# Optimization experiments

Measured on AMD Instinct MI355X. Metric: run time of the kernel, lower is better.

## Reference

```python
import jax, jax.numpy as jnp
import numpy as np

D_MODEL = 1024
N_HEADS = 16
HEAD_DIM = D_MODEL // N_HEADS
MAX_REL = 1024
BATCH = 4
SEQ = 1024


def setup_inputs() -> dict:
    key = jax.random.key(0)
    ks = jax.random.split(key, 12)
    f32 = jnp.float32
    scale = 0.02
    inp = {
        "query": jax.random.normal(ks[0], (BATCH, SEQ, D_MODEL), f32),
        "key": jax.random.normal(ks[1], (BATCH, SEQ, D_MODEL), f32),
        "value": jax.random.normal(ks[2], (BATCH, SEQ, D_MODEL), f32),
        # causal mask: 1 indicates positions to mask (strict upper triangle)
        "attention_mask": jnp.triu(jnp.ones((SEQ, SEQ), jnp.int32), k=1)[None, None],
        "Wq": jax.random.normal(ks[3], (D_MODEL, D_MODEL), f32) * scale,
        "bq": jnp.zeros((D_MODEL,), f32),
        "Wk": jax.random.normal(ks[4], (D_MODEL, D_MODEL), f32) * scale,
        "bk": jnp.zeros((D_MODEL,), f32),
        "Wv": jax.random.normal(ks[5], (D_MODEL, D_MODEL), f32) * scale,
        "bv": jnp.zeros((D_MODEL,), f32),
        "rel_tab": jax.random.normal(ks[6], (MAX_REL, D_MODEL), f32) * scale,
        "Wo": jax.random.normal(ks[7], (D_MODEL, D_MODEL), f32) * scale,
        "bo": jnp.zeros((D_MODEL,), f32),
    }
    return inp


def _relative_positions(rel_tab, seq_len):
    # Mirrors get_relative_positions with max_len = MAX_REL (static ints).
    pad_n = max(seq_len - MAX_REL, 0)
    start = max(MAX_REL - seq_len, 0)
    tail = rel_tab[start:MAX_REL]  # (min(seq_len, MAX_REL), D)
    if pad_n > 0:
        head = jnp.tile(rel_tab[0:1], (pad_n, 1))
        return jnp.concatenate([head, tail], axis=0)
    return tail  # (seq_len, D)


def _skew(pos_raw):
    # pos_raw: (B, H, S, S). Music-Transformer skew trick:
    # pad one column on the left, reshape, drop first row, reshape back.
    B, H, Sq, Sk = pos_raw.shape
    padded = jnp.pad(pos_raw, ((0, 0), (0, 0), (0, 0), (1, 0)))  # (B,H,Sq,Sk+1)
    t = padded.reshape(-1, Sk + 1, Sq)
    return t[:, 1:].reshape(B, H, Sq, Sk)


def reference(query, key, value, attention_mask, Wq, bq, Wk, bk, Wv, bv, rel_tab, Wo, bo):
    B, Sq, D = query.shape
    Sk = key.shape[-2]
    H, hd = N_HEADS, HEAD_DIM

    q = query @ Wq + bq
    k = key @ Wk + bk
    v = value @ Wv + bv
    rel = _relative_positions(rel_tab, Sk)  # (Sk, D)

    # split heads -> (B, H, S, hd); rel -> (H, Sk, hd)
    qh = q.reshape(B, Sq, H, hd).transpose(0, 2, 1, 3)
    kh = k.reshape(B, Sk, H, hd).transpose(0, 2, 1, 3)
    vh = v.reshape(B, Sk, H, hd).transpose(0, 2, 1, 3)
    rh = rel.reshape(Sk, H, hd).transpose(1, 0, 2)

    content = jnp.einsum('bhqd,bhkd->bhqk', qh, kh)
    pos_raw = jnp.einsum('bhqd,hkd->bhqk', qh, rh)
    pos = _skew(pos_raw)

    scale = 1.0 / np.sqrt(hd).astype(np.float32)
    scores = (content + pos) * scale
    scores = jnp.where(attention_mask == 1, jnp.float32(-1e9), scores)
    weights = jax.nn.softmax(scores, axis=-1)

    out = jnp.einsum('bhqk,bhkd->bhqd', weights, vh)
    out = out.transpose(0, 2, 1, 3).reshape(B, Sq, D)
    return out @ Wo + bo
```

## Files before the change

kernel.cpp:

```cpp
#include <hip/hip_runtime.h>
#include <cstddef>
#include <cstdint>


typedef __attribute__((ext_vector_type(8))) short bf16x8;
typedef __attribute__((ext_vector_type(4))) float f32x4;
typedef __attribute__((ext_vector_type(4))) unsigned int u32x4;

using u16 = unsigned short;
using u32 = unsigned int;

#define QSCALE (0.125f * 1.44269504089f)

__device__ __forceinline__ f32x4 mfma16(bf16x8 a, bf16x8 b, f32x4 c) {
  return __builtin_amdgcn_mfma_f32_16x16x32_bf16(a, b, c, 0, 0, 0);
}
__device__ __forceinline__ u32 fbits(float f) {
  union { float f; u32 u; } v; v.f = f; return v.u;
}
__device__ __forceinline__ float uif(u32 u) {
  union { u32 u; float f; } v; v.u = u; return v.f;
}
__device__ __forceinline__ u16 f2b(float f) { return (u16)((fbits(f) + 0x8000u) >> 16); }
__device__ __forceinline__ u32 pack2(float a, float b) {
  return ((fbits(a) + 0x8000u) >> 16) | ((fbits(b) + 0x8000u) & 0xffff0000u);
}
__device__ __forceinline__ float b2f(u16 u) {
  union { u32 i; float f; } v; v.i = ((u32)u) << 16; return v.f;
}
__device__ __forceinline__ float exp2_fast(float x) {
  float r; asm("v_exp_f32 %0, %1" : "=v"(r) : "v"(x)); return r;
}
__device__ __forceinline__ void gload16(const void* g, void* l) {
  __builtin_amdgcn_global_load_lds(
      (const __attribute__((address_space(1))) u32*)g,
      (__attribute__((address_space(3))) u32*)l, 16, 0, 0);
}

__global__ __launch_bounds__(256) void cvt_qkv(
    const float* __restrict__ a0, const float* __restrict__ a1,
    const float* __restrict__ a2, u16* __restrict__ o0,
    u16* __restrict__ o1, u16* __restrict__ o2) {
  int z = blockIdx.y;
  const float* src = (z == 0) ? a0 : (z == 1) ? a1 : a2;
  u16* dst = (z == 0) ? o0 : (z == 1) ? o1 : o2;
  size_t i = ((size_t)blockIdx.x * 256 + threadIdx.x) * 4;
  f32x4 v = *(const f32x4*)(src + i);
  uint2 pk; pk.x = pack2(v[0], v[1]); pk.y = pack2(v[2], v[3]);
  *(uint2*)(dst + i) = pk;
}

__global__ __launch_bounds__(256) void prep(
    const float* __restrict__ Wq, const float* __restrict__ Wk,
    const float* __restrict__ Wv, const float* __restrict__ rel,
    u16* __restrict__ WqT, u16* __restrict__ WkT, u16* __restrict__ WvT,
    u16* __restrict__ relb) {
  __shared__ __align__(16) u16 tile[64][65];
  int z = blockIdx.z;
  if (z == 3) {
    int blk = blockIdx.y * 16 + blockIdx.x;
    size_t base = (size_t)blk * 4096;
#pragma unroll
    for (int e = 0; e < 4; e++) {
      size_t idx = base + e * 1024 + threadIdx.x * 4;
      f32x4 v = *(const f32x4*)(rel + idx);
      uint2 pk; pk.x = pack2(v[0], v[1]); pk.y = pack2(v[2], v[3]);
      *(uint2*)(relb + idx) = pk;
    }
    return;
  }
  const float* W = (z == 0) ? Wq : (z == 1) ? Wk : Wv;
  u16* T = (z == 0) ? WqT : (z == 1) ? WkT : WvT;
  float sc = (z == 0) ? QSCALE : 1.0f;
  int k0 = blockIdx.x * 64, n0 = blockIdx.y * 64;
  for (int e = threadIdx.x; e < 4096; e += 256) {
    int r = e >> 6, c = e & 63;
    tile[r][c] = f2b(sc * W[(size_t)(k0 + r) * 1024 + n0 + c]);
  }
  __syncthreads();
  for (int e = threadIdx.x; e < 4096; e += 256) {
    int r = e >> 6, c = e & 63;
    T[(size_t)(n0 + r) * 1024 + k0 + c] = tile[c][r];
  }
}

__global__ __launch_bounds__(256) void transpose_wo(
    const float* __restrict__ W, u16* __restrict__ T) {
  __shared__ __align__(16) u16 tile[64][65];
  int k0 = blockIdx.x * 64, n0 = blockIdx.y * 64;
  for (int e = threadIdx.x; e < 4096; e += 256) {
    int r = e >> 6, c = e & 63;
    tile[r][c] = f2b(W[(size_t)(k0 + r) * 1024 + n0 + c]);
  }
  __syncthreads();
  for (int e = threadIdx.x; e < 4096; e += 256) {
    int r = e >> 6, c = e & 63;
    T[(size_t)(n0 + r) * 1024 + k0 + c] = tile[c][r];
  }
}

__device__ __forceinline__ void gemm_epilogue(
    f32x4 (&acc)[4][4], const float* __restrict__ bias, float bscale,
    void* __restrict__ Cv, int layout, int m0, int n0, int wr, int wc,
    int quad, int ln) {
#pragma unroll
  for (int ct = 0; ct < 4; ct++) {
    int n = n0 + wc + 16 * ct + ln;
    float bs = bscale * bias[n];
#pragma unroll
    for (int rt = 0; rt < 4; rt++) {
#pragma unroll
      for (int r = 0; r < 4; r++) {
        int m = m0 + wr + 16 * rt + quad * 4 + r;
        float v = acc[rt][ct][r] + bs;
        if (layout == 0) {
          ((float*)Cv)[(size_t)m * 1024 + n] = v;
        } else {
          int b_ = m >> 10, s = m & 1023, h = n >> 6, d = n & 63;
          size_t idx = (layout == 1)
              ? ((size_t)(b_ * 16 + h) * 1024 + s) * 64 + d
              : ((size_t)(b_ * 16 + h) * 64 + d) * 1024 + s;
          ((u16*)Cv)[idx] = f2b(v);
        }
      }
    }
  }
}

__device__ __forceinline__ void gemm_glds_body(
    const u16* __restrict__ A, const u16* __restrict__ Bt,
    const float* __restrict__ bias, float bscale, void* __restrict__ Cv,
    int layout) {
  __shared__ __align__(16) u16 As[128 * 64];
  __shared__ __align__(16) u16 Bs[128 * 64];
  int m0 = blockIdx.x * 128, n0 = blockIdx.y * 128;
  int tid = threadIdx.x;
  int w = tid >> 6, lane = tid & 63, quad = lane >> 4, ln = lane & 15;
  int wr = (w >> 1) * 64, wc = (w & 1) * 64;

  int rowin = lane >> 3;
  int swz = ((lane & 7) ^ rowin) * 8;

  f32x4 acc[4][4];
#pragma unroll
  for (int i = 0; i < 4; i++)
#pragma unroll
    for (int j = 0; j < 4; j++) { acc[i][j][0]=0.f; acc[i][j][1]=0.f; acc[i][j][2]=0.f; acc[i][j][3]=0.f; }

  const u16* aA = A  + (size_t)(m0 + 32 * w + rowin) * 1024 + swz;
  const u16* aB = Bt + (size_t)(n0 + 32 * w + rowin) * 1024 + swz;

  for (int k0 = 0; k0 < 1024; k0 += 64) {
#pragma unroll
    for (int j = 0; j < 4; j++) {
      gload16(aA + k0 + (size_t)(8 * j) * 1024, &As[(32 * w + 8 * j) * 64]);
      gload16(aB + k0 + (size_t)(8 * j) * 1024, &Bs[(32 * w + 8 * j) * 64]);
    }
    __syncthreads();
#pragma unroll
    for (int kk = 0; kk < 64; kk += 32) {
      int sA = (((quad + (kk >> 3)) ^ (ln & 7))) * 8;
      bf16x8 af[4], bfr[4];
#pragma unroll
      for (int rt = 0; rt < 4; rt++)
        af[rt] = *(const bf16x8*)&As[(wr + 16 * rt + ln) * 64 + sA];
#pragma unroll
      for (int ct = 0; ct < 4; ct++)
        bfr[ct] = *(const bf16x8*)&Bs[(wc + 16 * ct + ln) * 64 + sA];
#pragma unroll
      for (int rt = 0; rt < 4; rt++)
#pragma unroll
        for (int ct = 0; ct < 4; ct++)
          acc[rt][ct] = mfma16(af[rt], bfr[ct], acc[rt][ct]);
    }
    __syncthreads();
  }

  gemm_epilogue(acc, bias, bscale, Cv, layout, m0, n0, wr, wc, quad, ln);
}

__device__ __forceinline__ void gemm128_body_f32(
    const float* __restrict__ Av, const u16* __restrict__ Bt,
    const float* __restrict__ bias, float bscale, void* __restrict__ Cv,
    int layout) {
  __shared__ __align__(16) u16 As[128][72];
  __shared__ __align__(16) u16 Bs[128][72];
  int m0 = blockIdx.x * 128, n0 = blockIdx.y * 128;
  int tid = threadIdx.x;
  int w = tid >> 6, lane = tid & 63, quad = lane >> 4, ln = lane & 15;
  int wr = (w >> 1) * 64, wc = (w & 1) * 64;
  int sr = tid >> 1, seg = (tid & 1) * 32;

  f32x4 acc[4][4];
#pragma unroll
  for (int i = 0; i < 4; i++)
#pragma unroll
    for (int j = 0; j < 4; j++) { acc[i][j][0]=0.f; acc[i][j][1]=0.f; acc[i][j][2]=0.f; acc[i][j][3]=0.f; }

  for (int k0 = 0; k0 < 1024; k0 += 64) {
    {
      const float* ap = Av + (size_t)(m0 + sr) * 1024 + k0 + seg;
      u32 pk[16];
#pragma unroll
      for (int j = 0; j < 8; j++) {
        f32x4 v = *(const f32x4*)(ap + 4 * j);
        pk[2 * j]     = pack2(v[0], v[1]);
        pk[2 * j + 1] = pack2(v[2], v[3]);
      }
      u32* d = (u32*)&As[sr][seg];
#pragma unroll
      for (int j = 0; j < 4; j++) *(u32x4*)(d + 4 * j) = *(u32x4*)(pk + 4 * j);
    }
    {
      const u16* bp = Bt + (size_t)(n0 + sr) * 1024 + k0 + seg;
#pragma unroll
      for (int j = 0; j < 4; j++)
        *(bf16x8*)&Bs[sr][seg + 8 * j] = *(const bf16x8*)(bp + 8 * j);
    }
    __syncthreads();
#pragma unroll
    for (int kk = 0; kk < 64; kk += 32) {
      bf16x8 af[4], bfr[4];
#pragma unroll
      for (int rt = 0; rt < 4; rt++)
        af[rt] = *(const bf16x8*)&As[wr + 16 * rt + ln][kk + quad * 8];
#pragma unroll
      for (int ct = 0; ct < 4; ct++)
        bfr[ct] = *(const bf16x8*)&Bs[wc + 16 * ct + ln][kk + quad * 8];
#pragma unroll
      for (int rt = 0; rt < 4; rt++)
#pragma unroll
        for (int ct = 0; ct < 4; ct++)
          acc[rt][ct] = mfma16(af[rt], bfr[ct], acc[rt][ct]);
    }
    __syncthreads();
  }

  gemm_epilogue(acc, bias, bscale, Cv, layout, m0, n0, wr, wc, quad, ln);
}

__global__ __launch_bounds__(256) void gemm_qkv_f32(
    const float* q, const float* k, const float* v, const u16* WT,
    const float* bq, const float* bk, const float* bv,
    u16* Qp, u16* Kp, u16* Vt) {
  int z = blockIdx.z;
  const float* A = (z == 0) ? q : (z == 1) ? k : v;
  const u16* Bt = WT + (size_t)z * (1024 * 1024);
  const float* bias = (z == 0) ? bq : (z == 1) ? bk : bv;
  float bscale = (z == 0) ? QSCALE : 1.0f;
  void* C = (z == 0) ? (void*)Qp : (z == 1) ? (void*)Kp : (void*)Vt;
  gemm128_body_f32(A, Bt, bias, bscale, C, (z == 2) ? 2 : 1);
}

__global__ __launch_bounds__(256) void gemm_qkv_bf(
    const u16* qb, const u16* kb, const u16* vb, const u16* WT,
    const float* bq, const float* bk, const float* bv,
    u16* Qp, u16* Kp, u16* Vt) {
  int z = blockIdx.z;
  const u16* A = (z == 0) ? qb : (z == 1) ? kb : vb;
  const u16* Bt = WT + (size_t)z * (1024 * 1024);
  const float* bias = (z == 0) ? bq : (z == 1) ? bk : bv;
  float bscale = (z == 0) ? QSCALE : 1.0f;
  void* C = (z == 0) ? (void*)Qp : (z == 1) ? (void*)Kp : (void*)Vt;
  gemm_glds_body(A, Bt, bias, bscale, C, (z == 2) ? 2 : 1);
}

__global__ __launch_bounds__(256) void gemm_out(
    const u16* A, const u16* Bt, const float* bias, float* C) {
  gemm_glds_body(A, Bt, bias, 1.0f, C, 0);
}

#define PSTRIDE 280

__global__ __launch_bounds__(256, 3) void attn_v2(
    const u16* __restrict__ Q, const u16* __restrict__ K,
    const u16* __restrict__ Vt, const u16* __restrict__ RB,
    u16* __restrict__ att) {
  __shared__ __align__(16) u16 lP[64 * PSTRIDE];

  int bh = blockIdx.x;
  int qt = 15 - blockIdx.y;
  int b = bh >> 4, h = bh & 15;
  int tid = threadIdx.x;
  int w = tid >> 6, lane = tid & 63, quad = lane >> 4, ln = lane & 15;

  const u16* Qb = Q + (size_t)bh * 65536;
  const u16* Kb = K + (size_t)bh * 65536;
  const u16* Vb = Vt + (size_t)bh * 65536;
  const u16* Rb = RB + h * 64;

  int row0 = 16 * w + quad * 4;
  int i0 = qt * 64;
  int R0f = 960 - i0;

  int vaddr[4];
  bool cond[4];
#pragma unroll
  for (int r = 0; r < 4; r++) {
    int Kq = 15 - 4 * quad - r;
    vaddr[r] = (((lane & 48) | ((Kq + ln) & 15))) << 2;
    cond[r] = (Kq + ln) >= 16;
  }

  int qrow = i0 + 16 * w + ln;
  bf16x8 qa0 = *(const bf16x8*)(Qb + (size_t)qrow * 64 + quad * 8);
  bf16x8 qa1 = *(const bf16x8*)(Qb + (size_t)qrow * 64 + 32 + quad * 8);

  bf16x8 ones;
#pragma unroll
  for (int i = 0; i < 8; i++) ones[i] = (short)0x3F80;

  f32x4 o[4], lacc;
#pragma unroll
  for (int c = 0; c < 4; c++) { o[c][0]=0.f; o[c][1]=0.f; o[c][2]=0.f; o[c][3]=0.f; }
  lacc[0]=0.f; lacc[1]=0.f; lacc[2]=0.f; lacc[3]=0.f;

#pragma unroll 1
  for (int js = 0; js <= i0; js += 256) {
    int ntiles = ((i0 - js) >> 6) + 1;
    if (ntiles > 4) ntiles = 4;
    int borig = R0f + js + 48 - 16 * w;

    f32x4 prev;
    {
      int rrow = borig + ln;
      int rl = rrow > 1023 ? 1023 : rrow;
      const u16* Rrow = Rb + (size_t)rl * 1024 + quad * 8;
      f32x4 a; a[0]=0.f; a[1]=0.f; a[2]=0.f; a[3]=0.f;
      a = mfma16(qa0, *(const bf16x8*)(Rrow), a);
      a = mfma16(qa1, *(const bf16x8*)(Rrow + 32), a);
#pragma unroll
      for (int r = 0; r < 4; r++)
        prev[r] = uif((u32)__builtin_amdgcn_ds_bpermute(vaddr[r], (int)fbits(a[r])));
    }

#pragma unroll
    for (int t = 0; t < 4; t++) {
      if (t < ntiles) {
        u32 Bp[4][2];
#pragma unroll
        for (int u = 0; u < 4; u++) {
          int m = 4 * t + 1 + u;
          int rrow = borig + 16 * m + ln;
          int rl = rrow > 1023 ? 1023 : rrow;
          const u16* Rrow = Rb + (size_t)rl * 1024 + quad * 8;
          f32x4 a; a[0]=0.f; a[1]=0.f; a[2]=0.f; a[3]=0.f;
          a = mfma16(qa0, *(const bf16x8*)(Rrow), a);
          a = mfma16(qa1, *(const bf16x8*)(Rrow + 32), a);
          f32x4 rot;
#pragma unroll
          for (int r = 0; r < 4; r++)
            rot[r] = uif((u32)__builtin_amdgcn_ds_bpermute(vaddr[r], (int)fbits(a[r])));
          float b0 = cond[0] ? rot[0] : prev[0];
          float b1 = cond[1] ? rot[1] : prev[1];
          float b2 = cond[2] ? rot[2] : prev[2];
          float b3 = cond[3] ? rot[3] : prev[3];
          Bp[u][0] = pack2(b0, b1);
          Bp[u][1] = pack2(b2, b3);
          prev = rot;
        }

        int j0 = js + 64 * t;
        bf16x8 kf[4][2];
#pragma unroll
        for (int c = 0; c < 4; c++) {
          const u16* Krow = Kb + (size_t)(j0 + 16 * c + ln) * 64 + quad * 8;
          kf[c][0] = *(const bf16x8*)(Krow);
          kf[c][1] = *(const bf16x8*)(Krow + 32);
        }
        f32x4 sc[4];
#pragma unroll
        for (int c = 0; c < 4; c++) {
          f32x4 a; a[0]=0.f; a[1]=0.f; a[2]=0.f; a[3]=0.f;
          a = mfma16(qa0, kf[c][0], a);
          a = mfma16(qa1, kf[c][1], a);
          sc[c] = a;
        }
        bool diag = (j0 == i0);
#pragma unroll
        for (int c = 0; c < 4; c++) {
          u32 pk0 = Bp[c][0];
          u32 pk1 = Bp[c][1];
          int jj = 16 * c + ln;
#pragma unroll
          for (int r = 0; r < 4; r++) {
            u16 bv = (u16)((r == 0) ? pk0 : (r == 1) ? (pk0 >> 16)
                           : (r == 2) ? pk1 : (pk1 >> 16));
            float s = sc[c][r] + b2f(bv);
            int ii = row0 + r;
            float p = (diag && jj > ii) ? 0.f : exp2_fast(s);
            lP[ii * PSTRIDE + 64 * t + jj] = f2b(p);
          }
        }
      }
    }
    asm volatile("s_waitcnt lgkmcnt(0)" ::: "memory");

    int KC = 2 * ntiles;
#pragma unroll 1
    for (int kc = 0; kc < KC; kc++) {
      bf16x8 pa = *(const bf16x8*)&lP[(16 * w + ln) * PSTRIDE + 32 * kc + quad * 8];
      lacc = mfma16(pa, ones, lacc);
#pragma unroll
      for (int c = 0; c < 4; c++) {
        const u16* Vrow = Vb + (size_t)(16 * c + ln) * 1024 + js + 32 * kc + quad * 8;
        o[c] = mfma16(pa, *(const bf16x8*)(Vrow), o[c]);
      }
    }
    asm volatile("s_waitcnt lgkmcnt(0)" ::: "memory");
  }

#pragma unroll
  for (int c = 0; c < 4; c++) {
#pragma unroll
    for (int r = 0; r < 4; r++) {
      int i_abs = i0 + row0 + r;
      att[((size_t)(b * 1024 + i_abs)) * 1024 + h * 64 + 16 * c + ln] =
          f2b(o[c][r] / lacc[r]);
    }
  }
}

extern "C" void kernel_launch(void* const* d_in, const int* in_sizes, int n_in,
                              void* d_out, int out_size, void* d_ws, size_t ws_size,
                              hipStream_t stream) {
  const float* query = (const float*)d_in[0];
  const float* key   = (const float*)d_in[1];
  const float* value = (const float*)d_in[2];
  const float* Wq = (const float*)d_in[4];
  const float* bq = (const float*)d_in[5];
  const float* Wk = (const float*)d_in[6];
  const float* bk = (const float*)d_in[7];
  const float* Wv = (const float*)d_in[8];
  const float* bv = (const float*)d_in[9];
  const float* RT = (const float*)d_in[10];
  const float* Wo = (const float*)d_in[11];
  const float* bo = (const float*)d_in[12];
  float* out = (float*)d_out;

  const size_t EM = 1024 * 1024;
  u16* ws   = (u16*)d_ws;
  u16* WT   = ws;
  u16* relb = ws + 3 * EM;
  u16* Kp   = ws + 4 * EM;
  u16* Vtp  = ws + 8 * EM;
  u16* Qp   = (u16*)d_out;
  u16* WoT  = ws;

  prep<<<dim3(16, 16, 4), 256, 0, stream>>>(Wq, Wk, Wv, RT,
                                            WT, WT + EM, WT + 2 * EM, relb);

  if (ws_size >= (size_t)48 * 1024 * 1024) {
    u16* qb = ws + 12 * EM;
    u16* kb = ws + 16 * EM;
    u16* vb = ws + 20 * EM;
    cvt_qkv<<<dim3(4096, 3), 256, 0, stream>>>(query, key, value, qb, kb, vb);
    gemm_qkv_bf<<<dim3(32, 8, 3), 256, 0, stream>>>(qb, kb, vb, WT,
                                                    bq, bk, bv, Qp, Kp, Vtp);
    u16* attw = ws + 12 * EM;
    attn_v2<<<dim3(64, 16), 256, 0, stream>>>(Qp, Kp, Vtp, relb, attw);
    transpose_wo<<<dim3(16, 16), 256, 0, stream>>>(Wo, WoT);
    gemm_out<<<dim3(32, 8), 256, 0, stream>>>(attw, WoT, bo, out);
  } else {
    gemm_qkv_f32<<<dim3(32, 8, 3), 256, 0, stream>>>(query, key, value, WT,
                                                     bq, bk, bv, Qp, Kp, Vtp);
    u16* attb = (u16*)d_out + 4 * EM;
    u16* attc = ws + 4 * EM;
    attn_v2<<<dim3(64, 16), 256, 0, stream>>>(Qp, Kp, Vtp, relb, attb);
    hipMemcpyAsync(attc, attb, 8 * 1024 * 1024, hipMemcpyDeviceToDevice, stream);
    transpose_wo<<<dim3(16, 16), 256, 0, stream>>>(Wo, WoT);
    gemm_out<<<dim3(32, 8), 256, 0, stream>>>(attc, WoT, bo, out);
  }
}
```

Baseline: 298.9 us.

## Split attention key range across two blocks and merge partial outputs

Replaces the single attention kernel with a split-K variant: each query tile is processed by two blocks handling interleaved 256-key chunks, each writing unnormalized bf16 partial outputs and row sums. A new merge kernel sums the partials and normalizes before the output projection. This doubles the grid to improve occupancy and balance the causal workload. It adds a merge pass with extra global traffic and stores partial outputs in bf16, which costs some precision. The Wo transpose is moved ahead of attention.

```diff
diff --git a/kernel.cpp b/kernel.cpp
--- a/kernel.cpp
+++ b/kernel.cpp
@@ -271,6 +271,188 @@
 }
 
 #define PSTRIDE 280
+
+__global__ __launch_bounds__(256, 3) void attn_split(
+    const u16* __restrict__ Q, const u16* __restrict__ K,
+    const u16* __restrict__ Vt, const u16* __restrict__ RB,
+    u16* __restrict__ po, float* __restrict__ plc) {
+  __shared__ __align__(16) u16 lP[64 * PSTRIDE];
+
+  int bh = blockIdx.x;
+  int yy = blockIdx.y;
+  int qt = 15 - (yy >> 1);
+  int half = yy & 1;
+  int h = bh & 15;
+  int tid = threadIdx.x;
+  int w = tid >> 6, lane = tid & 63, quad = lane >> 4, ln = lane & 15;
+
+  const u16* Qb = Q + (size_t)bh * 65536;
+  const u16* Kb = K + (size_t)bh * 65536;
+  const u16* Vb = Vt + (size_t)bh * 65536;
+  const u16* Rb = RB + h * 64;
+
+  int row0 = 16 * w + quad * 4;
+  int i0 = qt * 64;
+  int R0f = 960 - i0;
+
+  int vaddr[4];
+  bool cond[4];
+#pragma unroll
+  for (int r = 0; r < 4; r++) {
+    int Kq = 15 - 4 * quad - r;
+    vaddr[r] = (((lane & 48) | ((Kq + ln) & 15))) << 2;
+    cond[r] = (Kq + ln) >= 16;
+  }
+
+  int qrow = i0 + 16 * w + ln;
+  bf16x8 qa0 = *(const bf16x8*)(Qb + (size_t)qrow * 64 + quad * 8);
+  bf16x8 qa1 = *(const bf16x8*)(Qb + (size_t)qrow * 64 + 32 + quad * 8);
+
+  bf16x8 ones;
+#pragma unroll
+  for (int i = 0; i < 8; i++) ones[i] = (short)0x3F80;
+
+  f32x4 o[4], lacc;
+#pragma unroll
+  for (int c = 0; c < 4; c++) { o[c][0]=0.f; o[c][1]=0.f; o[c][2]=0.f; o[c][3]=0.f; }
+  lacc[0]=0.f; lacc[1]=0.f; lacc[2]=0.f; lacc[3]=0.f;
+
+#pragma unroll 1
+  for (int js = half * 256; js <= i0; js += 512) {
+    int ntiles = ((i0 - js) >> 6) + 1;
+    if (ntiles > 4) ntiles = 4;
+    int borig = R0f + js + 48 - 16 * w;
+
+    f32x4 prev;
+    {
+      int rrow = borig + ln;
+      int rl = rrow > 1023 ? 1023 : rrow;
+      const u16* Rrow = Rb + (size_t)rl * 1024 + quad * 8;
+      f32x4 a; a[0]=0.f; a[1]=0.f; a[2]=0.f; a[3]=0.f;
+      a = mfma16(qa0, *(const bf16x8*)(Rrow), a);
+      a = mfma16(qa1, *(const bf16x8*)(Rrow + 32), a);
+#pragma unroll
+      for (int r = 0; r < 4; r++)
+        prev[r] = uif((u32)__builtin_amdgcn_ds_bpermute(vaddr[r], (int)fbits(a[r])));
+    }
+
+#pragma unroll
+    for (int t = 0; t < 4; t++) {
+      if (t < ntiles) {
+        u32 Bp[4][2];
+#pragma unroll
+        for (int u = 0; u < 4; u++) {
+          int m = 4 * t + 1 + u;
+          int rrow = borig + 16 * m + ln;
+          int rl = rrow > 1023 ? 1023 : rrow;
+          const u16* Rrow = Rb + (size_t)rl * 1024 + quad * 8;
+          f32x4 a; a[0]=0.f; a[1]=0.f; a[2]=0.f; a[3]=0.f;
+          a = mfma16(qa0, *(const bf16x8*)(Rrow), a);
+          a = mfma16(qa1, *(const bf16x8*)(Rrow + 32), a);
+          f32x4 rot;
+#pragma unroll
+          for (int r = 0; r < 4; r++)
+            rot[r] = uif((u32)__builtin_amdgcn_ds_bpermute(vaddr[r], (int)fbits(a[r])));
+          float b0 = cond[0] ? rot[0] : prev[0];
+          float b1 = cond[1] ? rot[1] : prev[1];
+          float b2 = cond[2] ? rot[2] : prev[2];
+          float b3 = cond[3] ? rot[3] : prev[3];
+          Bp[u][0] = pack2(b0, b1);
+          Bp[u][1] = pack2(b2, b3);
+          prev = rot;
+        }
+
+        int j0 = js + 64 * t;
+        bf16x8 kf[4][2];
+#pragma unroll
+        for (int c = 0; c < 4; c++) {
+          const u16* Krow = Kb + (size_t)(j0 + 16 * c + ln) * 64 + quad * 8;
+          kf[c][0] = *(const bf16x8*)(Krow);
+          kf[c][1] = *(const bf16x8*)(Krow + 32);
+        }
+        f32x4 sc[4];
+#pragma unroll
+        for (int c = 0; c < 4; c++) {
+          f32x4 a; a[0]=0.f; a[1]=0.f; a[2]=0.f; a[3]=0.f;
+          a = mfma16(qa0, kf[c][0], a);
+          a = mfma16(qa1, kf[c][1], a);
+          sc[c] = a;
+        }
+        bool diag = (j0 == i0);
+#pragma unroll
+        for (int c = 0; c < 4; c++) {
+          u32 pk0 = Bp[c][0];
+          u32 pk1 = Bp[c][1];
+          int jj = 16 * c + ln;
+#pragma unroll
+          for (int r = 0; r < 4; r++) {
+            u16 bv = (u16)((r == 0) ? pk0 : (r == 1) ? (pk0 >> 16)
+                           : (r == 2) ? pk1 : (pk1 >> 16));
+            float s = sc[c][r] + b2f(bv);
+            int ii = row0 + r;
+            float p = (diag && jj > ii) ? 0.f : exp2_fast(s);
+            lP[ii * PSTRIDE + 64 * t + jj] = f2b(p);
+          }
+        }
+      }
+    }
+    asm volatile("s_waitcnt lgkmcnt(0)" ::: "memory");
+
+    int KC = 2 * ntiles;
+#pragma unroll 1
+    for (int kc = 0; kc < KC; kc++) {
+      bf16x8 pa = *(const bf16x8*)&lP[(16 * w + ln) * PSTRIDE + 32 * kc + quad * 8];
+      lacc = mfma16(pa, ones, lacc);
+#pragma unroll
+      for (int c = 0; c < 4; c++) {
+        const u16* Vrow = Vb + (size_t)(16 * c + ln) * 1024 + js + 32 * kc + quad * 8;
+        o[c] = mfma16(pa, *(const bf16x8*)(Vrow), o[c]);
+      }
+    }
+    asm volatile("s_waitcnt lgkmcnt(0)" ::: "memory");
+  }
+
+  size_t slot = ((size_t)(bh * 16 + qt) * 2 + half);
+  u16* pob = po + slot * 4096;
+#pragma unroll
+  for (int c = 0; c < 4; c++) {
+#pragma unroll
+    for (int r = 0; r < 4; r++)
+      pob[(row0 + r) * 64 + 16 * c + ln] = f2b(o[c][r]);
+  }
+  if (ln == 0) {
+#pragma unroll
+    for (int r = 0; r < 4; r++)
+      plc[slot * 64 + row0 + r] = lacc[r];
+  }
+}
+
+__global__ __launch_bounds__(256) void merge_att(
+    const u16* __restrict__ po, const float* __restrict__ plc,
+    u16* __restrict__ att) {
+  int bh = blockIdx.x, qt = blockIdx.y;
+  int b = bh >> 4, h = bh & 15;
+  int tid = threadIdx.x;
+  int row = tid >> 2, cs = (tid & 3) * 16;
+  size_t sl = (size_t)(bh * 16 + qt) * 2;
+  const u16* p0 = po + sl * 4096 + row * 64 + cs;
+  const u16* p1 = p0 + 4096;
+  float l = plc[sl * 64 + row] + plc[sl * 64 + 64 + row];
+  float inv = 1.0f / l;
+  __align__(16) u16 outv[16];
+#pragma unroll
+  for (int g = 0; g < 2; g++) {
+    bf16x8 a = *(const bf16x8*)(p0 + 8 * g);
+    bf16x8 c = *(const bf16x8*)(p1 + 8 * g);
+#pragma unroll
+    for (int j = 0; j < 8; j++)
+      outv[8 * g + j] = f2b((b2f((u16)a[j]) + b2f((u16)c[j])) * inv);
+  }
+  int i_abs = qt * 64 + row;
+  u16* dst = att + ((size_t)(b * 1024 + i_abs)) * 1024 + h * 64 + cs;
+  *(u32x4*)(dst) = *(const u32x4*)(outv);
+  *(u32x4*)(dst + 8) = *(const u32x4*)(outv + 8);
+}
 
 __global__ __launch_bounds__(256, 3) void attn_v2(
     const u16* __restrict__ Q, const u16* __restrict__ K,
@@ -457,9 +639,12 @@
     cvt_qkv<<<dim3(4096, 3), 256, 0, stream>>>(query, key, value, qb, kb, vb);
     gemm_qkv_bf<<<dim3(32, 8, 3), 256, 0, stream>>>(qb, kb, vb, WT,
                                                     bq, bk, bv, Qp, Kp, Vtp);
+    transpose_wo<<<dim3(16, 16), 256, 0, stream>>>(Wo, WoT);
+    u16*   po  = ws + 16 * EM;
+    float* plc = (float*)(ws + 2 * EM);
+    attn_split<<<dim3(64, 32), 256, 0, stream>>>(Qp, Kp, Vtp, relb, po, plc);
     u16* attw = ws + 12 * EM;
-    attn_v2<<<dim3(64, 16), 256, 0, stream>>>(Qp, Kp, Vtp, relb, attw);
-    transpose_wo<<<dim3(16, 16), 256, 0, stream>>>(Wo, WoT);
+    merge_att<<<dim3(64, 16), 256, 0, stream>>>(po, plc, attw);
     gemm_out<<<dim3(32, 8), 256, 0, stream>>>(attw, WoT, bo, out);
   } else {
     gemm_qkv_f32<<<dim3(32, 8, 3), 256, 0, stream>>>(query, key, value, WT,
```

New measurement: 309.8 us. +3.6%, slower.

## Stage V tiles in swizzled LDS via direct global-to-LDS loads in attention

Applied to the files above, without the earlier changes.

Each attention block now copies its 64x256 slice of transposed V into a new shared buffer with direct global-to-LDS loads and an XOR column swizzle. The PV MFMAs then read V from LDS with the matching swizzle instead of issuing strided global loads, and the waits become block barriers. The extra shared memory lowers the occupancy target from 3 to 2 blocks. The Wo transpose launch is also moved ahead of the attention kernel.

```diff
diff --git a/kernel.cpp b/kernel.cpp
--- a/kernel.cpp
+++ b/kernel.cpp
@@ -272,11 +272,16 @@
 
 #define PSTRIDE 280
 
-__global__ __launch_bounds__(256, 3) void attn_v2(
+__device__ __forceinline__ int cswz_row(int row) {
+  return (((row ^ (row >> 3)) & 7) << 3) ^ (((row >> 3) & 3) << 6);
+}
+
+__global__ __launch_bounds__(256, 2) void attn_v2(
     const u16* __restrict__ Q, const u16* __restrict__ K,
     const u16* __restrict__ Vt, const u16* __restrict__ RB,
     u16* __restrict__ att) {
   __shared__ __align__(16) u16 lP[64 * PSTRIDE];
+  __shared__ __align__(16) u16 lVs[64 * 256];
 
   int bh = blockIdx.x;
   int qt = 15 - blockIdx.y;
@@ -302,6 +307,16 @@
     cond[r] = (Kq + ln) >= 16;
   }
 
+  int vsrc[8];
+#pragma unroll
+  for (int j = 0; j < 8; j++) {
+    int arow = 16 * w + 2 * j + (lane >> 5);
+    vsrc[j] = arow * 1024 + (((lane & 31) * 8) ^ cswz_row(arow));
+  }
+  int cswz[4];
+#pragma unroll
+  for (int c = 0; c < 4; c++) cswz[c] = cswz_row(16 * c + ln);
+
   int qrow = i0 + 16 * w + ln;
   bf16x8 qa0 = *(const bf16x8*)(Qb + (size_t)qrow * 64 + quad * 8);
   bf16x8 qa1 = *(const bf16x8*)(Qb + (size_t)qrow * 64 + 32 + quad * 8);
@@ -320,6 +335,17 @@
     int ntiles = ((i0 - js) >> 6) + 1;
     if (ntiles > 4) ntiles = 4;
     int borig = R0f + js + 48 - 16 * w;
+
+#pragma unroll
+    for (int j = 0; j < 8; j++) {
+      int so = vsrc[j] + js;
+      int rowbase = (vsrc[j] >> 10);
+      (void)rowbase;
+      int arow = 16 * w + 2 * j + (lane >> 5);
+      int colp = so - arow * 1024;
+      if (colp > 1008) colp = 1008;
+      gload16(Vb + (size_t)arow * 1024 + colp, &lVs[(16 * w + 2 * j) * 256]);
+    }
 
     f32x4 prev;
     {
@@ -394,7 +420,7 @@
         }
       }
     }
-    asm volatile("s_waitcnt lgkmcnt(0)" ::: "memory");
+    __syncthreads();
 
     int KC = 2 * ntiles;
 #pragma unroll 1
@@ -403,11 +429,11 @@
       lacc = mfma16(pa, ones, lacc);
 #pragma unroll
       for (int c = 0; c < 4; c++) {
-        const u16* Vrow = Vb + (size_t)(16 * c + ln) * 1024 + js + 32 * kc + quad * 8;
-        o[c] = mfma16(pa, *(const bf16x8*)(Vrow), o[c]);
+        int col = (32 * kc + quad * 8) ^ cswz[c];
+        o[c] = mfma16(pa, *(const bf16x8*)&lVs[(16 * c + ln) * 256 + col], o[c]);
       }
     }
-    asm volatile("s_waitcnt lgkmcnt(0)" ::: "memory");
+    __syncthreads();
   }
 
 #pragma unroll
@@ -457,9 +483,9 @@
     cvt_qkv<<<dim3(4096, 3), 256, 0, stream>>>(query, key, value, qb, kb, vb);
     gemm_qkv_bf<<<dim3(32, 8, 3), 256, 0, stream>>>(qb, kb, vb, WT,
                                                     bq, bk, bv, Qp, Kp, Vtp);
+    transpose_wo<<<dim3(16, 16), 256, 0, stream>>>(Wo, WoT);
     u16* attw = ws + 12 * EM;
     attn_v2<<<dim3(64, 16), 256, 0, stream>>>(Qp, Kp, Vtp, relb, attw);
-    transpose_wo<<<dim3(16, 16), 256, 0, stream>>>(Wo, WoT);
     gemm_out<<<dim3(32, 8), 256, 0, stream>>>(attw, WoT, bo, out);
   } else {
     gemm_qkv_f32<<<dim3(32, 8, 3), 256, 0, stream>>>(query, key, value, WT,
```

Result: faster. 274.3 us (-8.2%).
